# Optimization experiments

Measured on AMD Instinct MI355X. Metric: run time of the kernel, lower is better.

Reference implementation:

```python
import jax, jax.numpy as jnp
import numpy as np
from jax import lax


def setup_inputs() -> dict:
    key = jax.random.key(0)
    ks = jax.random.split(key, 8)
    B, S, H, L = 64, 512, 768, 9
    hidden = jax.random.normal(ks[0], (B, S, H), jnp.float32)
    label = jax.random.randint(ks[1], (B, S), 0, L, dtype=jnp.int32)
    mask = jnp.ones((B, S), jnp.int32)
    W = jax.random.normal(ks[2], (H, L), jnp.float32) * 0.02
    b = jnp.zeros((L,), jnp.float32)
    start_transitions = jax.random.normal(ks[3], (L,), jnp.float32) * 0.1
    end_transitions = jax.random.normal(ks[4], (L,), jnp.float32) * 0.1
    transitions = jax.random.normal(ks[5], (L, L), jnp.float32) * 0.1
    return dict(hidden=hidden, label=label, mask=mask, W=W, b=b,
                start_transitions=start_transitions,
                end_transitions=end_transitions,
                transitions=transitions)


def reference(hidden, label, mask, W, b, start_transitions, end_transitions, transitions):
    B, S, H = hidden.shape
    L = b.shape[0]
    # output_layer: [B,S,H] @ [H,L] -> emissions, then transpose to time-major [S,B,L]
    emissions = jnp.einsum('bsh,hl->bsl', hidden, W) + b
    em = jnp.transpose(emissions, (1, 0, 2))        # [S, B, L]
    tags = label.T                                   # [S, B]
    m = mask.T.astype(jnp.float32)                   # [S, B]

    def gather_tag(em_t, tag_t):
        # em_t [B,L], tag_t [B] -> [B]
        return jnp.take_along_axis(em_t, tag_t[:, None], axis=1)[:, 0]

    # ---- numerator: score of the gold path ----
    score0 = start_transitions[tags[0]] + gather_tag(em[0], tags[0])
    def num_step(carry, x):
        score, prev = carry
        em_t, tag_t, m_t = x
        s = transitions[prev, tag_t] + gather_tag(em_t, tag_t)
        score = score + s * m_t
        prev = jnp.where(m_t > 0, tag_t, prev)
        return (score, prev), None
    (score, last_gold), _ = lax.scan(num_step, (score0, tags[0]), (em[1:], tags[1:], m[1:]))
    score = score + end_transitions[last_gold]

    # ---- denominator: forward algorithm (logsumexp DP) ----
    alpha0 = start_transitions[None, :] + em[0]      # [B, L]
    def fwd_step(alpha, x):
        em_t, m_t = x
        nxt = jax.nn.logsumexp(alpha[:, :, None] + transitions[None, :, :] + em_t[:, None, :], axis=1)
        alpha = jnp.where(m_t[:, None] > 0, nxt, alpha)
        return alpha, None
    alphaT, _ = lax.scan(fwd_step, alpha0, (em[1:], m[1:]))
    logZ = jax.nn.logsumexp(alphaT + end_transitions[None, :], axis=1)

    llh = jnp.sum(score - logZ)                      # reduction='sum'
    loss = -llh / B

    # ---- Viterbi decode (decode() is called without mask -> full length) ----
    v0 = start_transitions[None, :] + em[0]
    def vit_step(v, em_t):
        scores = v[:, :, None] + transitions[None, :, :] + em_t[:, None, :]  # [B, L, L]
        return jnp.max(scores, axis=1), jnp.argmax(scores, axis=1)
    vT, hist = lax.scan(vit_step, v0, em[1:])        # hist [S-1, B, L]
    last_tag = jnp.argmax(vT + end_transitions[None, :], axis=1)  # [B]
    def back_step(tag, bp_t):
        prev = jnp.take_along_axis(bp_t, tag[:, None], axis=1)[:, 0]
        return prev, prev
    _, prevs = lax.scan(back_step, last_tag, hist, reverse=True)  # [S-1, B]
    path = jnp.concatenate([prevs, last_tag[None, :]], axis=0).T  # [B, S]

    # ---- accuracy bookkeeping (label > 0 mask) ----
    label_flat = label.reshape(-1)
    label_mask = (label_flat > 0).astype(jnp.int32)
    predict = path.reshape(-1).astype(jnp.int32) * label_mask
    correct = jnp.sum((predict == label_flat).astype(jnp.float32))
    return loss, correct, predict, label_flat
```

## Files before the change

### kernel.cpp

```cpp
#include <hip/hip_runtime.h>
#include <hip/hip_bf16.h>

#define NB 64
#define NS 512
#define NH 768
#define NL 9
#define NROWS (NB*NS)
#define EMN (NROWS*NL)

__device__ __forceinline__ float readlane_f(float v, int l) {
    return __int_as_float(__builtin_amdgcn_readlane(__float_as_int(v), l));
}
__device__ __forceinline__ unsigned long long readlane_u64(unsigned long long v, int l) {
    unsigned int lo = (unsigned int)__builtin_amdgcn_readlane((int)(unsigned int)(v & 0xffffffffULL), l);
    unsigned int hi = (unsigned int)__builtin_amdgcn_readlane((int)(unsigned int)(v >> 32), l);
    return ((unsigned long long)hi << 32) | (unsigned long long)lo;
}
template <int CTRL>
__device__ __forceinline__ float dpp_add(float x) {
    int t = __builtin_amdgcn_update_dpp(0, __float_as_int(x), CTRL, 0xf, 0xf, false);
    return x + __int_as_float(t);
}
__device__ __forceinline__ float wave_sum_to63(float x) {
    x = dpp_add<0x111>(x);
    x = dpp_add<0x112>(x);
    x = dpp_add<0x114>(x);
    x = dpp_add<0x118>(x);
    x = dpp_add<0x142>(x);
    x = dpp_add<0x143>(x);
    return x;
}

__global__ __launch_bounds__(256) void k_gemm(const float* __restrict__ hidden,
                                              const float* __restrict__ W,
                                              const float* __restrict__ bias,
                                              float* __restrict__ em,
                                              float* __restrict__ out) {
    int tid = threadIdx.x;
    int lane = tid & 63;
    int w = blockIdx.x * 4 + (tid >> 6);
    if (blockIdx.x == 0 && tid == 0) { out[0] = 0.f; out[1] = 0.f; }

    float4 Wr[3][9];
    const float4* Wp = (const float4*)W;
#pragma unroll
    for (int c = 0; c < 3; c++) {
        const float4* p = Wp + 9 * lane + 576 * c;
#pragma unroll
        for (int q = 0; q < 9; q++) Wr[c][q] = p[q];
    }
    float bz[NL];
#pragma unroll
    for (int j = 0; j < NL; j++) bz[j] = bias[j];

#pragma unroll
    for (int r = 0; r < 4; r++) {
        int row = 4 * w + r;
        const float* hp = hidden + (size_t)row * NH;
        float4 h[3];
#pragma unroll
        for (int c = 0; c < 3; c++) h[c] = *(const float4*)(hp + 4 * lane + 256 * c);
        float acc[NL];
#pragma unroll
        for (int j = 0; j < NL; j++) acc[j] = 0.f;
#pragma unroll
        for (int c = 0; c < 3; c++) {
            const float hv[4] = { h[c].x, h[c].y, h[c].z, h[c].w };
#pragma unroll
            for (int kk = 0; kk < 4; kk++) {
#pragma unroll
                for (int j = 0; j < NL; j++) {
                    int fl = kk * 9 + j;
                    const float4& wq = Wr[c][fl >> 2];
                    float wv = (fl & 3) == 0 ? wq.x : (fl & 3) == 1 ? wq.y : (fl & 3) == 2 ? wq.z : wq.w;
                    acc[j] = fmaf(hv[kk], wv, acc[j]);
                }
            }
        }
        float s[NL];
#pragma unroll
        for (int j = 0; j < NL; j++) s[j] = wave_sum_to63(acc[j]);
        if (lane == 63) {
            float* o = em + (size_t)row * NL;
#pragma unroll
            for (int j = 0; j < NL; j++) o[j] = s[j] + bz[j];
        }
    }
}

__global__ __launch_bounds__(256) void k_dp(const float* __restrict__ em,
                                            const int* __restrict__ label,
                                            const int* __restrict__ mask,
                                            const float* __restrict__ startT,
                                            const float* __restrict__ endT,
                                            const float* __restrict__ trans,
                                            float* __restrict__ out) {
    __shared__ float s_em[NS * NL];
    __shared__ float s_v[NS * NL];
    __shared__ unsigned char s_bp[NS * NL];
    __shared__ unsigned char s_path[NS];
    __shared__ int s_mk[NS];
    __shared__ float s_T[NL * NL];

    int bx = blockIdx.x;
    int tid = threadIdx.x;
    int b = bx & 63;

    {
        const float4* ef = (const float4*)(em + (size_t)b * NS * NL);
        float4* sf = (float4*)s_em;
        for (int q = tid; q < NS * NL / 4; q += 256) sf[q] = ef[q];
        if (tid < NS / 4) ((int4*)s_mk)[tid] = ((const int4*)(mask + b * NS))[tid];
        if (tid < NL * NL) s_T[tid] = trans[tid];
    }
    __syncthreads();

    if (bx < NB) {
        if (tid < 64) {
            int j9 = tid < NL ? tid : NL - 1;
            float Mcol[NL];
#pragma unroll
            for (int i = 0; i < NL; i++) Mcol[i] = __expf(s_T[i * NL + j9]);
            float a = __expf(startT[j9] + s_em[j9]);
            int eacc = 0;
            float xpre[4]; int mpre[4];
#pragma unroll
            for (int p = 0; p < 4; p++) { xpre[p] = __expf(s_em[(1 + p) * NL + j9]); mpre[p] = s_mk[1 + p]; }
#pragma unroll 4
            for (int t = 1; t < NS; ++t) {
                float xev = xpre[0]; int mv = mpre[0];
                xpre[0] = xpre[1]; xpre[1] = xpre[2]; xpre[2] = xpre[3];
                mpre[0] = mpre[1]; mpre[1] = mpre[2]; mpre[2] = mpre[3];
                int tn = t + 4; tn = tn < NS ? tn : NS - 1;
                xpre[3] = __expf(s_em[tn * NL + j9]); mpre[3] = s_mk[tn];
                float p0 = readlane_f(a, 0) * Mcol[0];
                float p1 = readlane_f(a, 1) * Mcol[1];
                float p2 = readlane_f(a, 2) * Mcol[2];
                float p3 = readlane_f(a, 3) * Mcol[3];
                float p4 = readlane_f(a, 4) * Mcol[4];
                float p5 = readlane_f(a, 5) * Mcol[5];
                float p6 = readlane_f(a, 6) * Mcol[6];
                float p7 = readlane_f(a, 7) * Mcol[7];
                float p8 = readlane_f(a, 8) * Mcol[8];
                float s = (((p0 + p1) + (p2 + p3)) + ((p4 + p5) + (p6 + p7))) + p8;
                float anew = xev * s;
                a = (mv > 0) ? anew : a;
                if ((t & 7) == 0) {
                    float c0 = readlane_f(a, 0), c1 = readlane_f(a, 1), c2 = readlane_f(a, 2);
                    float c3 = readlane_f(a, 3), c4 = readlane_f(a, 4), c5 = readlane_f(a, 5);
                    float c6 = readlane_f(a, 6), c7 = readlane_f(a, 7), c8 = readlane_f(a, 8);
                    float c = (((c0 + c1) + (c2 + c3)) + ((c4 + c5) + (c6 + c7))) + c8;
                    int ex = ((__float_as_int(c) >> 23) & 255) - 127;
                    a = ldexpf(a, -ex);
                    eacc += ex;
                }
            }
            float z = a * __expf(endT[j9]);
            float c0 = readlane_f(z, 0), c1 = readlane_f(z, 1), c2 = readlane_f(z, 2);
            float c3 = readlane_f(z, 3), c4 = readlane_f(z, 4), c5 = readlane_f(z, 5);
            float c6 = readlane_f(z, 6), c7 = readlane_f(z, 7), c8 = readlane_f(z, 8);
            float c = (((c0 + c1) + (c2 + c3)) + ((c4 + c5) + (c6 + c7))) + c8;
            if (tid == 0) {
                float lz = (float)eacc * 0.6931471805599453f + __logf(c);
                atomicAdd(out, lz * (1.0f / (float)NB));
            }
        } else if (tid < 128) {
            int lane = tid & 63;
            const int* lb = label + b * NS;
            int t0 = lane * 8;
            int lab[8]; int mk[8];
#pragma unroll
            for (int r = 0; r < 8; r++) { lab[r] = lb[t0 + r]; mk[r] = s_mk[t0 + r]; }
            if (lane == 0) mk[0] = 1;
            int h = 0, sl = 0;
#pragma unroll
            for (int r = 0; r < 8; r++) { if (mk[r] > 0) { h = 1; sl = lab[r]; } }
#pragma unroll
            for (int d = 1; d < 64; d <<= 1) {
                int ho = __shfl_up(h, d);
                int so = __shfl_up(sl, d);
                if (!h) { h = ho; sl = so; }
            }
            int lg = __shfl(sl, 63);
            int incoming = __shfl_up(sl, 1);
            float sc = 0.f;
            int prevr = (lane == 0) ? lab[0] : incoming;
#pragma unroll
            for (int r = 0; r < 8; r++) {
                int t = t0 + r;
                if (t > 0) {
                    float s = s_T[prevr * NL + lab[r]] + s_em[t * NL + lab[r]];
                    sc += s * (float)mk[r];
                }
                if (mk[r] > 0) prevr = lab[r];
            }
            if (lane == 0) {
                int g0 = lab[0];
                sc += startT[g0] + s_em[g0] + endT[lg];
            }
#pragma unroll
            for (int d = 1; d < 64; d <<= 1) sc += __shfl_xor(sc, d);
            if (lane == 0) atomicAdd(out, -sc * (1.0f / (float)NB));
        }
    } else {
        if (tid < 64) {
            int j9 = tid < NL ? tid : NL - 1;
            float Tcol[NL];
#pragma unroll
            for (int i = 0; i < NL; i++) Tcol[i] = s_T[i * NL + j9];
            float v = startT[j9] + s_em[j9];
            if (tid < NL) s_v[tid] = v;
            float epre[4];
#pragma unroll
            for (int p = 0; p < 4; p++) epre[p] = s_em[(1 + p) * NL + j9];
#pragma unroll 4
            for (int t = 1; t < NS; ++t) {
                float emv = epre[0];
                epre[0] = epre[1]; epre[1] = epre[2]; epre[2] = epre[3];
                int tn = t + 4; tn = tn < NS ? tn : NS - 1;
                epre[3] = s_em[tn * NL + j9];
                float m0 = readlane_f(v, 0) + Tcol[0];
                float m1 = readlane_f(v, 1) + Tcol[1];
                float m2 = readlane_f(v, 2) + Tcol[2];
                float m3 = readlane_f(v, 3) + Tcol[3];
                float m4 = readlane_f(v, 4) + Tcol[4];
                float m5 = readlane_f(v, 5) + Tcol[5];
                float m6 = readlane_f(v, 6) + Tcol[6];
                float m7 = readlane_f(v, 7) + Tcol[7];
                float m8 = readlane_f(v, 8) + Tcol[8];
                float M = fmaxf(fmaxf(fmaxf(fmaxf(m0, m1), fmaxf(m2, m3)),
                                      fmaxf(fmaxf(m4, m5), fmaxf(m6, m7))), m8);
                v = M + emv;
                if (tid < NL) s_v[t * NL + tid] = v;
            }
        }
        __syncthreads();
#pragma unroll
        for (int rep = 0; rep < 2; rep++) {
            int t = 1 + tid + 256 * rep;
            if (t < NS) {
                float vp[NL], emt[NL];
#pragma unroll
                for (int i = 0; i < NL; i++) vp[i] = s_v[(t - 1) * NL + i];
#pragma unroll
                for (int j = 0; j < NL; j++) emt[j] = s_em[t * NL + j];
#pragma unroll
                for (int j = 0; j < NL; j++) {
                    float e = emt[j];
                    float val[NL];
#pragma unroll
                    for (int i = 0; i < NL; i++) val[i] = (vp[i] + s_T[i * NL + j]) + e;
                    bool c01 = val[0] >= val[1]; float m01 = c01 ? val[0] : val[1]; int i01 = c01 ? 0 : 1;
                    bool c23 = val[2] >= val[3]; float m23 = c23 ? val[2] : val[3]; int i23 = c23 ? 2 : 3;
                    bool c45 = val[4] >= val[5]; float m45 = c45 ? val[4] : val[5]; int i45 = c45 ? 4 : 5;
                    bool c67 = val[6] >= val[7]; float m67 = c67 ? val[6] : val[7]; int i67 = c67 ? 6 : 7;
                    bool ca = m01 >= m23; float ma = ca ? m01 : m23; int ia = ca ? i01 : i23;
                    bool cb = m45 >= m67; float mb = cb ? m45 : m67; int ib = cb ? i45 : i67;
                    bool cc = ma >= mb;  float mc = cc ? ma : mb;  int ic = cc ? ia : ib;
                    bool cd = mc >= val[8]; int bi = cd ? ic : 8;
                    s_bp[t * NL + j] = (unsigned char)bi;
                }
            } else if (t == NS) {
                s_bp[0 * NL + tid - 255] = 0;
            }
        }
        __syncthreads();
        if (tid < 64) {
            int lane = tid;
            float bb = s_v[(NS - 1) * NL + 0] + endT[0]; int lt = 0;
#pragma unroll
            for (int jj = 1; jj < NL; jj++) {
                float fj = s_v[(NS - 1) * NL + jj] + endT[jj];
                if (fj > bb) { bb = fj; lt = jj; }
            }
            unsigned long long G[8];
#pragma unroll
            for (int r = 0; r < 8; r++) {
                int t0 = (lane * 8 + r) * NL;
                unsigned long long g = 0;
                if (lane == 0 && r == 0) {
                    g = 0x876543210ULL;
                } else {
#pragma unroll
                    for (int x = 0; x < NL; x++) g |= (unsigned long long)s_bp[t0 + x] << (4 * x);
                }
                G[r] = g;
            }
            unsigned long long A = 0x876543210ULL;
#pragma unroll
            for (int r = 7; r >= 0; r--) {
                unsigned long long An = 0;
#pragma unroll
                for (int x = 0; x < NL; x++) {
                    int ax = (int)((A >> (4 * x)) & 15ULL);
                    int gv = (int)((G[r] >> (4 * ax)) & 15ULL);
                    An |= (unsigned long long)gv << (4 * x);
                }
                A = An;
            }
            int e = 0; int cur = lt;
            for (int ll = 63; ll >= 0; --ll) {
                if (lane == ll) e = cur;
                unsigned long long Al = readlane_u64(A, ll);
                cur = (int)((Al >> (4 * cur)) & 15ULL);
            }
            unsigned long long pw = 0; int c2 = e;
#pragma unroll
            for (int r = 7; r >= 0; r--) {
                pw |= (unsigned long long)c2 << (8 * r);
                c2 = (int)((G[r] >> (4 * c2)) & 15ULL);
            }
            *(unsigned long long*)(s_path + lane * 8) = pw;
        }
        __syncthreads();
        const int* lb = label + b * NS;
        float cnt = 0.f;
#pragma unroll
        for (int q = 0; q < 2; q++) {
            int t = tid + q * 256;
            int idx = b * NS + t;
            int lab = lb[t];
            int p = (int)s_path[t];
            int pred = (lab > 0) ? p : 0;
            out[2 + idx] = (float)pred;
            out[2 + NROWS + idx] = (float)lab;
            cnt += (pred == lab) ? 1.f : 0.f;
        }
#pragma unroll
        for (int d = 1; d < 64; d <<= 1) cnt += __shfl_xor(cnt, d);
        if ((tid & 63) == 0) atomicAdd(out + 1, cnt);
    }
}

extern "C" void kernel_launch(void* const* d_in, const int* in_sizes, int n_in,
                              void* d_out, int out_size, void* d_ws, size_t ws_size,
                              hipStream_t stream) {
    const float* hidden = (const float*)d_in[0];
    const int*   label  = (const int*)d_in[1];
    const int*   mask   = (const int*)d_in[2];
    const float* W      = (const float*)d_in[3];
    const float* bias   = (const float*)d_in[4];
    const float* startT = (const float*)d_in[5];
    const float* endT   = (const float*)d_in[6];
    const float* trans  = (const float*)d_in[7];
    float* out = (float*)d_out;

    float* em = (float*)d_ws;

    k_gemm<<<2048, 256, 0, stream>>>(hidden, W, bias, em, out);
    k_dp<<<128, 256, 0, stream>>>(em, label, mask, startT, endT, trans, out);
}
```

Measured before the change: 216.9 us.

## Fuse GEMM and CRF DP kernels with an atomic-counter grid barrier

Merges the emission GEMM kernel and the CRF forward/Viterbi kernel into one launch. Each block publishes completion through a global atomic counter, and the first 128 blocks spin until every GEMM block has finished before running the DP. The aim is to remove the second kernel launch and the gap between launches. In exchange, every block now reserves the DP's large shared-memory footprint, which can lower GEMM occupancy. The 128 spinning blocks also hold CU slots, and an extra memset is added to reset the counter.

```diff
diff --git a/kernel.cpp b/kernel.cpp
--- a/kernel.cpp
+++ b/kernel.cpp
@@ -7,6 +7,7 @@
 #define NL 9
 #define NROWS (NB*NS)
 #define EMN (NROWS*NL)
+#define NBLK 2048
 
 __device__ __forceinline__ float readlane_f(float v, int l) {
     return __int_as_float(__builtin_amdgcn_readlane(__float_as_int(v), l));
@@ -31,70 +32,17 @@
     return x;
 }
 
-__global__ __launch_bounds__(256) void k_gemm(const float* __restrict__ hidden,
-                                              const float* __restrict__ W,
-                                              const float* __restrict__ bias,
-                                              float* __restrict__ em,
-                                              float* __restrict__ out) {
-    int tid = threadIdx.x;
-    int lane = tid & 63;
-    int w = blockIdx.x * 4 + (tid >> 6);
-    if (blockIdx.x == 0 && tid == 0) { out[0] = 0.f; out[1] = 0.f; }
-
-    float4 Wr[3][9];
-    const float4* Wp = (const float4*)W;
-#pragma unroll
-    for (int c = 0; c < 3; c++) {
-        const float4* p = Wp + 9 * lane + 576 * c;
-#pragma unroll
-        for (int q = 0; q < 9; q++) Wr[c][q] = p[q];
-    }
-    float bz[NL];
-#pragma unroll
-    for (int j = 0; j < NL; j++) bz[j] = bias[j];
-
-#pragma unroll
-    for (int r = 0; r < 4; r++) {
-        int row = 4 * w + r;
-        const float* hp = hidden + (size_t)row * NH;
-        float4 h[3];
-#pragma unroll
-        for (int c = 0; c < 3; c++) h[c] = *(const float4*)(hp + 4 * lane + 256 * c);
-        float acc[NL];
-#pragma unroll
-        for (int j = 0; j < NL; j++) acc[j] = 0.f;
-#pragma unroll
-        for (int c = 0; c < 3; c++) {
-            const float hv[4] = { h[c].x, h[c].y, h[c].z, h[c].w };
-#pragma unroll
-            for (int kk = 0; kk < 4; kk++) {
-#pragma unroll
-                for (int j = 0; j < NL; j++) {
-                    int fl = kk * 9 + j;
-                    const float4& wq = Wr[c][fl >> 2];
-                    float wv = (fl & 3) == 0 ? wq.x : (fl & 3) == 1 ? wq.y : (fl & 3) == 2 ? wq.z : wq.w;
-                    acc[j] = fmaf(hv[kk], wv, acc[j]);
-                }
-            }
-        }
-        float s[NL];
-#pragma unroll
-        for (int j = 0; j < NL; j++) s[j] = wave_sum_to63(acc[j]);
-        if (lane == 63) {
-            float* o = em + (size_t)row * NL;
-#pragma unroll
-            for (int j = 0; j < NL; j++) o[j] = s[j] + bz[j];
-        }
-    }
-}
-
-__global__ __launch_bounds__(256) void k_dp(const float* __restrict__ em,
-                                            const int* __restrict__ label,
-                                            const int* __restrict__ mask,
-                                            const float* __restrict__ startT,
-                                            const float* __restrict__ endT,
-                                            const float* __restrict__ trans,
-                                            float* __restrict__ out) {
+__global__ __launch_bounds__(256) void k_fused(const float* __restrict__ hidden,
+                                               const float* __restrict__ W,
+                                               const float* __restrict__ bias,
+                                               const int* __restrict__ label,
+                                               const int* __restrict__ mask,
+                                               const float* __restrict__ startT,
+                                               const float* __restrict__ endT,
+                                               const float* __restrict__ trans,
+                                               float* __restrict__ em,
+                                               unsigned int* __restrict__ ctr,
+                                               float* __restrict__ out) {
     __shared__ float s_em[NS * NL];
     __shared__ float s_v[NS * NL];
     __shared__ unsigned char s_bp[NS * NL];
@@ -104,8 +52,76 @@
 
     int bx = blockIdx.x;
     int tid = threadIdx.x;
+    int lane = tid & 63;
+
+    {
+        int w = bx * 4 + (tid >> 6);
+        if (bx == 0 && tid == 0) { out[0] = 0.f; out[1] = 0.f; }
+        float4 Wr[3][9];
+        const float4* Wp = (const float4*)W;
+#pragma unroll
+        for (int c = 0; c < 3; c++) {
+            const float4* p = Wp + 9 * lane + 576 * c;
+#pragma unroll
+            for (int q = 0; q < 9; q++) Wr[c][q] = p[q];
+        }
+        float bz[NL];
+#pragma unroll
+        for (int j = 0; j < NL; j++) bz[j] = bias[j];
+
+#pragma unroll
+        for (int r = 0; r < 4; r++) {
+            int row = 4 * w + r;
+            const float* hp = hidden + (size_t)row * NH;
+            float4 h[3];
+#pragma unroll
+            for (int c = 0; c < 3; c++) h[c] = *(const float4*)(hp + 4 * lane + 256 * c);
+            float acc[NL];
+#pragma unroll
+            for (int j = 0; j < NL; j++) acc[j] = 0.f;
+#pragma unroll
+            for (int c = 0; c < 3; c++) {
+                const float hv[4] = { h[c].x, h[c].y, h[c].z, h[c].w };
+#pragma unroll
+                for (int kk = 0; kk < 4; kk++) {
+#pragma unroll
+                    for (int j = 0; j < NL; j++) {
+                        int fl = kk * 9 + j;
+                        const float4& wq = Wr[c][fl >> 2];
+                        float wv = (fl & 3) == 0 ? wq.x : (fl & 3) == 1 ? wq.y : (fl & 3) == 2 ? wq.z : wq.w;
+                        acc[j] = fmaf(hv[kk], wv, acc[j]);
+                    }
+                }
+            }
+            float s[NL];
+#pragma unroll
+            for (int j = 0; j < NL; j++) s[j] = wave_sum_to63(acc[j]);
+            if (lane == 63) {
+                float* o = em + (size_t)row * NL;
+#pragma unroll
+                for (int j = 0; j < NL; j++) o[j] = s[j] + bz[j];
+            }
+        }
+    }
+
+    __syncthreads();
+    if (tid == 0) {
+        __threadfence();
+        __atomic_fetch_add(ctr, 1u, __ATOMIC_RELEASE);
+    }
+    if (bx >= 128) return;
+
+    if (tid == 0) {
+        long long guard = 0;
+        while (__hip_atomic_load(ctr, __ATOMIC_ACQUIRE, __HIP_MEMORY_SCOPE_AGENT) < NBLK) {
+            __builtin_amdgcn_s_sleep(2);
+            if (++guard > (1LL << 34)) break;
+        }
+        __threadfence();
+    }
+    __syncthreads();
+
     int b = bx & 63;
-
     {
         const float4* ef = (const float4*)(em + (size_t)b * NS * NL);
         float4* sf = (float4*)s_em;
@@ -165,7 +181,6 @@
                 atomicAdd(out, lz * (1.0f / (float)NB));
             }
         } else if (tid < 128) {
-            int lane = tid & 63;
             const int* lb = label + b * NS;
             int t0 = lane * 8;
             int lab[8]; int mk[8];
@@ -266,7 +281,6 @@
         }
         __syncthreads();
         if (tid < 64) {
-            int lane = tid;
             float bb = s_v[(NS - 1) * NL + 0] + endT[0]; int lt = 0;
 #pragma unroll
             for (int jj = 1; jj < NL; jj++) {
@@ -346,7 +360,9 @@
     float* out = (float*)d_out;
 
     float* em = (float*)d_ws;
-
-    k_gemm<<<2048, 256, 0, stream>>>(hidden, W, bias, em, out);
-    k_dp<<<128, 256, 0, stream>>>(em, label, mask, startT, endT, trans, out);
-}
+    unsigned int* ctr = (unsigned int*)((float*)d_ws + EMN);
+
+    hipMemsetAsync(ctr, 0, sizeof(unsigned int), stream);
+    k_fused<<<NBLK, 256, 0, stream>>>(hidden, W, bias, label, mask,
+                                      startT, endT, trans, em, ctr, out);
+}
```

Result: slower. 471.6 us (+117.4%).

## Split GEMM K dimension across four waves with shared-memory reduction

Applied to the files above, without the earlier changes.

The emission GEMM now gives each block 4 rows and splits the 768-wide K dimension across its 4 waves. Each lane loads 3 scalar hidden values with stride-64 coalesced access and holds only 27 W values in registers, where it used to hold 108. Wave partial sums are combined through shared memory, and the grid grows from 2048 to 8192 blocks. The aim is to cut register pressure, raise occupancy and memory-level parallelism on this bandwidth-bound read of hidden, at the cost of extra syncs, more reductions per row and scalar loads in place of float4 loads.

```diff
diff --git a/kernel.cpp b/kernel.cpp
--- a/kernel.cpp
+++ b/kernel.cpp
@@ -36,55 +36,45 @@
                                               const float* __restrict__ bias,
                                               float* __restrict__ em,
                                               float* __restrict__ out) {
+    __shared__ float s_part[4][4][NL];
     int tid = threadIdx.x;
     int lane = tid & 63;
-    int w = blockIdx.x * 4 + (tid >> 6);
-    if (blockIdx.x == 0 && tid == 0) { out[0] = 0.f; out[1] = 0.f; }
-
-    float4 Wr[3][9];
-    const float4* Wp = (const float4*)W;
+    int w = tid >> 6;
+    int bx = blockIdx.x;
+    if (bx == 0 && tid == 0) { out[0] = 0.f; out[1] = 0.f; }
+
+    int kbase = 192 * w + lane;
+    float Wv[3][NL];
 #pragma unroll
     for (int c = 0; c < 3; c++) {
-        const float4* p = Wp + 9 * lane + 576 * c;
-#pragma unroll
-        for (int q = 0; q < 9; q++) Wr[c][q] = p[q];
-    }
-    float bz[NL];
-#pragma unroll
-    for (int j = 0; j < NL; j++) bz[j] = bias[j];
+        const float* wp = W + (size_t)(kbase + 64 * c) * NL;
+#pragma unroll
+        for (int j = 0; j < NL; j++) Wv[c][j] = wp[j];
+    }
 
 #pragma unroll
     for (int r = 0; r < 4; r++) {
-        int row = 4 * w + r;
-        const float* hp = hidden + (size_t)row * NH;
-        float4 h[3];
-#pragma unroll
-        for (int c = 0; c < 3; c++) h[c] = *(const float4*)(hp + 4 * lane + 256 * c);
+        int row = 4 * bx + r;
+        const float* hp = hidden + (size_t)row * NH + kbase;
+        float h0 = hp[0], h1 = hp[64], h2 = hp[128];
         float acc[NL];
 #pragma unroll
-        for (int j = 0; j < NL; j++) acc[j] = 0.f;
-#pragma unroll
-        for (int c = 0; c < 3; c++) {
-            const float hv[4] = { h[c].x, h[c].y, h[c].z, h[c].w };
-#pragma unroll
-            for (int kk = 0; kk < 4; kk++) {
-#pragma unroll
-                for (int j = 0; j < NL; j++) {
-                    int fl = kk * 9 + j;
-                    const float4& wq = Wr[c][fl >> 2];
-                    float wv = (fl & 3) == 0 ? wq.x : (fl & 3) == 1 ? wq.y : (fl & 3) == 2 ? wq.z : wq.w;
-                    acc[j] = fmaf(hv[kk], wv, acc[j]);
-                }
-            }
-        }
-        float s[NL];
-#pragma unroll
-        for (int j = 0; j < NL; j++) s[j] = wave_sum_to63(acc[j]);
+        for (int j = 0; j < NL; j++) {
+            acc[j] = fmaf(h0, Wv[0][j], fmaf(h1, Wv[1][j], h2 * Wv[2][j]));
+        }
+#pragma unroll
+        for (int j = 0; j < NL; j++) acc[j] = wave_sum_to63(acc[j]);
         if (lane == 63) {
-            float* o = em + (size_t)row * NL;
-#pragma unroll
-            for (int j = 0; j < NL; j++) o[j] = s[j] + bz[j];
-        }
+#pragma unroll
+            for (int j = 0; j < NL; j++) s_part[w][r][j] = acc[j];
+        }
+    }
+    __syncthreads();
+    if (tid < 36) {
+        int r = tid / NL, j = tid % NL;
+        float v = (s_part[0][r][j] + s_part[1][r][j]) +
+                  (s_part[2][r][j] + s_part[3][r][j]) + bias[j];
+        em[(size_t)(4 * bx + r) * NL + j] = v;
     }
 }
 
@@ -104,6 +94,7 @@
 
     int bx = blockIdx.x;
     int tid = threadIdx.x;
+    int lane = tid & 63;
     int b = bx & 63;
 
     {
@@ -165,7 +156,6 @@
                 atomicAdd(out, lz * (1.0f / (float)NB));
             }
         } else if (tid < 128) {
-            int lane = tid & 63;
             const int* lb = label + b * NS;
             int t0 = lane * 8;
             int lab[8]; int mk[8];
@@ -266,7 +256,6 @@
         }
         __syncthreads();
         if (tid < 64) {
-            int lane = tid;
             float bb = s_v[(NS - 1) * NL + 0] + endT[0]; int lt = 0;
 #pragma unroll
             for (int jj = 1; jj < NL; jj++) {
@@ -347,6 +336,6 @@
 
     float* em = (float*)d_ws;
 
-    k_gemm<<<2048, 256, 0, stream>>>(hidden, W, bias, em, out);
+    k_gemm<<<8192, 256, 0, stream>>>(hidden, W, bias, em, out);
     k_dp<<<128, 256, 0, stream>>>(em, label, mask, startT, endT, trans, out);
 }
```

Measured after the change: 214.6 us. Within noise of the previous version (-1.1%).
